# Kernel tuning notes

Measured on AMD Instinct MI355X. Metric: run time of the kernel, lower is better.

Reference implementation:

```python
import jax, jax.numpy as jnp
import numpy as np

EMBED_DIM = 1024
NUM_HEADS = 16
HEAD_DIM = EMBED_DIM // NUM_HEADS
SCALE = HEAD_DIM ** -0.5


def setup_inputs() -> dict:
    key = jax.random.key(0)
    ks = jax.random.split(key, 12)
    B, S, D = 4, 2048, EMBED_DIM
    s = 0.02
    return {
        "query": jax.random.normal(ks[0], (B, S, D), jnp.float32),
        "key": jax.random.normal(ks[1], (B, S, D), jnp.float32),
        "value": jax.random.normal(ks[2], (B, S, D), jnp.float32),
        "Wq": jax.random.normal(ks[3], (D, D), jnp.float32) * s,
        "bq": jnp.zeros((D,), jnp.float32),
        "Wk": jax.random.normal(ks[4], (D, D), jnp.float32) * s,
        "bk": jnp.zeros((D,), jnp.float32),
        "Wv": jax.random.normal(ks[5], (D, D), jnp.float32) * s,
        "bv": jnp.zeros((D,), jnp.float32),
        "Wo": jax.random.normal(ks[6], (D, D), jnp.float32) * s,
        "bo": jnp.zeros((D,), jnp.float32),
    }


def reference(query, key, value, Wq, bq, Wk, bk, Wv, bv, Wo, bo):
    B, S, D = query.shape
    H, Hd = NUM_HEADS, HEAD_DIM

    # Linear projections (torch Linear: x @ W^T + b)
    q = query @ Wq.T + bq
    k = key @ Wk.T + bk
    v = value @ Wv.T + bv

    # [B, H, S, Hd]
    q = q.reshape(B, S, H, Hd).transpose(0, 2, 1, 3)
    k = k.reshape(B, -1, H, Hd).transpose(0, 2, 1, 3)
    v = v.reshape(B, -1, H, Hd).transpose(0, 2, 1, 3)

    # scores: [B, H, S, Skv]
    scores = jnp.einsum("bhsd,bhtd->bhst", q, k) * SCALE

    # is_causal=True: mask strictly upper triangle
    Skv = k.shape[2]
    causal = jnp.triu(jnp.ones((S, Skv), dtype=bool), k=1)
    scores = jnp.where(causal, -jnp.inf, scores)

    attn = jax.nn.softmax(scores, axis=-1)
    out = jnp.einsum("bhst,bhtd->bhsd", attn, v)  # [B, H, S, Hd]
    out = out.transpose(0, 2, 1, 3).reshape(B, S, D)
    output = out @ Wo.T + bo

    # need_weights=True, average_attn_weights=True -> mean over heads
    attn_weights = attn.mean(axis=1)  # [B, S, Skv]
    return output, attn_weights
```

## Files before the change

kernel.cpp:

```cpp
#include <hip/hip_runtime.h>
#include <hip/hip_bf16.h>
#include <cmath>

#define BC     4
#define SEQ    2048
#define DMODEL 1024
#define NHEAD  16
#define HD     64
#define ASCALE 0.125f
#define LOG2E  1.44269504f

typedef __bf16 bf16x8 __attribute__((ext_vector_type(8)));
typedef __bf16 bf16x4 __attribute__((ext_vector_type(4)));
typedef float  f32x4  __attribute__((ext_vector_type(4)));

__device__ __forceinline__ f32x4 mfma16x16x32(bf16x8 a, bf16x8 b, f32x4 c) {
    return __builtin_amdgcn_mfma_f32_16x16x32_bf16(a, b, c, 0, 0, 0);
}

__device__ __forceinline__ float fexp2(float x) {
    return __builtin_amdgcn_exp2f(x);
}

__device__ __forceinline__ void gload_lds16(const __bf16* g, __bf16* l) {
    __builtin_amdgcn_global_load_lds(
        (const __attribute__((address_space(1))) void*)g,
        (__attribute__((address_space(3))) void*)l, 16, 0, 0);
}

__global__ __launch_bounds__(256) void cvt_qkv(const float* __restrict__ a,
                                               const float* __restrict__ b,
                                               const float* __restrict__ c,
                                               __bf16* __restrict__ oa,
                                               __bf16* __restrict__ ob,
                                               __bf16* __restrict__ oc) {
    const float* in; __bf16* out;
    if (blockIdx.y == 0)      { in = a; out = oa; }
    else if (blockIdx.y == 1) { in = b; out = ob; }
    else                      { in = c; out = oc; }
    const size_t i = ((size_t)blockIdx.x * 256 + threadIdx.x) * 8;
    float4 f0 = *(const float4*)(in + i);
    float4 f1 = *(const float4*)(in + i + 4);
    bf16x8 o;
    o[0] = (__bf16)f0.x; o[1] = (__bf16)f0.y; o[2] = (__bf16)f0.z; o[3] = (__bf16)f0.w;
    o[4] = (__bf16)f1.x; o[5] = (__bf16)f1.y; o[6] = (__bf16)f1.z; o[7] = (__bf16)f1.w;
    *(bf16x8*)(out + i) = o;
}

__global__ __launch_bounds__(256) void cvt_w(const float* __restrict__ a,
                                             const float* __restrict__ b,
                                             const float* __restrict__ c,
                                             const float* __restrict__ d,
                                             __bf16* __restrict__ oa,
                                             __bf16* __restrict__ ob,
                                             __bf16* __restrict__ oc,
                                             __bf16* __restrict__ od) {
    const float* in; __bf16* out;
    if (blockIdx.y == 0)      { in = a; out = oa; }
    else if (blockIdx.y == 1) { in = b; out = ob; }
    else if (blockIdx.y == 2) { in = c; out = oc; }
    else                      { in = d; out = od; }
    const size_t i = ((size_t)blockIdx.x * 256 + threadIdx.x) * 8;
    float4 f0 = *(const float4*)(in + i);
    float4 f1 = *(const float4*)(in + i + 4);
    bf16x8 o;
    o[0] = (__bf16)f0.x; o[1] = (__bf16)f0.y; o[2] = (__bf16)f0.z; o[3] = (__bf16)f0.w;
    o[4] = (__bf16)f1.x; o[5] = (__bf16)f1.y; o[6] = (__bf16)f1.z; o[7] = (__bf16)f1.w;
    *(bf16x8*)(out + i) = o;
}

template <typename TO, bool VT>
__global__ __launch_bounds__(256) void gemm_bt16(const __bf16* __restrict__ A,
                                                 const __bf16* __restrict__ W,
                                                 const float* __restrict__ bias,
                                                 TO* __restrict__ out,
                                                 float scale) {
    constexpr int K = DMODEL, N = DMODEL;
    __shared__ __bf16 As[128 * 64];
    __shared__ __bf16 Bs[128 * 64];
    const int tid = threadIdx.x;
    const int lane = tid & 63;
    const int wid = tid >> 6;
    const int lr = lane & 15;
    const int lg = lane >> 4;
    const int wr = (wid >> 1) * 64;
    const int wc = (wid & 1) * 64;
    const int bm = blockIdx.x * 128;
    const int bn = blockIdx.y * 128;

    f32x4 acc[4][4] = {};

    for (int k0 = 0; k0 < K; k0 += 64) {
        #pragma unroll
        for (int i = 0; i < 4; ++i) {
            const int p = tid + 256 * i;
            const int row = p >> 3, c = p & 7;
            const int csrc = ((c ^ (row & 7)) * 8);
            gload_lds16(A + (size_t)(bm + row) * K + k0 + csrc, &As[p * 8]);
            gload_lds16(W + (size_t)(bn + row) * K + k0 + csrc, &Bs[p * 8]);
        }
        __syncthreads();

        #pragma unroll
        for (int kk = 0; kk < 2; ++kk) {
            bf16x8 af[4], bfg[4];
            #pragma unroll
            for (int m = 0; m < 4; ++m) {
                const int row = wr + m * 16 + lr;
                af[m] = *(const bf16x8*)&As[row * 64 + ((kk * 4 + lg) ^ (row & 7)) * 8];
            }
            #pragma unroll
            for (int n = 0; n < 4; ++n) {
                const int row = wc + n * 16 + lr;
                bfg[n] = *(const bf16x8*)&Bs[row * 64 + ((kk * 4 + lg) ^ (row & 7)) * 8];
            }
            #pragma unroll
            for (int m = 0; m < 4; ++m)
                #pragma unroll
                for (int n = 0; n < 4; ++n)
                    acc[m][n] = mfma16x16x32(af[m], bfg[n], acc[m][n]);
        }
        __syncthreads();
    }

    #pragma unroll
    for (int n = 0; n < 4; ++n) {
        const int col = bn + wc + n * 16 + lr;
        const float bb = bias[col];
        #pragma unroll
        for (int m = 0; m < 4; ++m) {
            const int row0 = bm + wr + m * 16 + lg * 4;
            if constexpr (VT) {
                const int h = col >> 6, hd = col & 63;
                const int b = row0 >> 11, s = row0 & 2047;
                bf16x4 pk;
                #pragma unroll
                for (int r = 0; r < 4; ++r) pk[r] = (__bf16)((acc[m][n][r] + bb) * scale);
                *(bf16x4*)((__bf16*)out + (((size_t)b * NHEAD + h) * HD + hd) * SEQ + s) = pk;
            } else {
                #pragma unroll
                for (int r = 0; r < 4; ++r)
                    out[(size_t)(row0 + r) * N + col] = (TO)((acc[m][n][r] + bb) * scale);
            }
        }
    }
}

__global__ __launch_bounds__(256) void flash_fwd(const __bf16* __restrict__ q,
                                                 const __bf16* __restrict__ k,
                                                 const __bf16* __restrict__ vt,
                                                 __bf16* __restrict__ o,
                                                 float* __restrict__ mbuf,
                                                 float* __restrict__ lbuf) {
    __shared__ __bf16 Ks[2][64][64];
    __shared__ __bf16 Vs[2][64][64];
    __shared__ __bf16 Ps[4][16][64];
    const int tid = threadIdx.x;
    const int lane = tid & 63;
    const int wid = tid >> 6;
    const int lr = lane & 15;
    const int lg = lane >> 4;

    const int flat = blockIdx.x;
    const int slot = flat >> 3;
    const int group = (flat & 7) * 8 + (slot >> 5);
    const int b = group >> 4;
    const int h = group & 15;
    const int qt = 31 - (slot & 31);

    const int qr = qt * 64 + wid * 16;
    const int myq = qr + lr;

    bf16x8 qf0, qf1;
    {
        const __bf16* qp = q + (size_t)(b * SEQ + myq) * DMODEL + h * HD + lg * 8;
        qf0 = ((const bf16x8*)qp)[0];
        qf1 = *(const bf16x8*)(qp + 32);
    }

    float m_run = -INFINITY;
    float l_run = 0.f;
    f32x4 oacc[4] = {};

    const int srow = tid >> 2;
    const int sc = (tid & 3) * 2;
    const int swz0 = (sc ^ (srow & 7)) * 8;
    const int swz1 = ((sc + 1) ^ (srow & 7)) * 8;
    const int rsw = (lr & 7);
    const int nt = qt + 1;

    const __bf16* kbase = k + (size_t)(b * SEQ + srow) * DMODEL + h * HD + sc * 8;
    const __bf16* vbase = vt + ((size_t)(b * NHEAD + h) * HD + srow) * SEQ + sc * 8;

    {
        bf16x8 kr0 = ((const bf16x8*)kbase)[0];
        bf16x8 kr1 = *(const bf16x8*)(kbase + 8);
        bf16x8 vr0 = ((const bf16x8*)vbase)[0];
        bf16x8 vr1 = *(const bf16x8*)(vbase + 8);
        *(bf16x8*)&Ks[0][srow][swz0] = kr0;
        *(bf16x8*)&Ks[0][srow][swz1] = kr1;
        *(bf16x8*)&Vs[0][srow][swz0] = vr0;
        *(bf16x8*)&Vs[0][srow][swz1] = vr1;
    }
    __syncthreads();

    for (int t = 0; t < nt; ++t) {
        const int buf = t & 1;
        const bool pre = (t + 1 < nt);
        bf16x8 kr0, kr1, vr0, vr1;
        if (pre) {
            const __bf16* kp = kbase + (size_t)(t + 1) * 64 * DMODEL;
            kr0 = ((const bf16x8*)kp)[0];
            kr1 = *(const bf16x8*)(kp + 8);
            const __bf16* vp = vbase + (t + 1) * 64;
            vr0 = ((const bf16x8*)vp)[0];
            vr1 = *(const bf16x8*)(vp + 8);
        }

        f32x4 z[4];
        __builtin_amdgcn_s_setprio(1);
        #pragma unroll
        for (int ts = 0; ts < 4; ++ts) {
            bf16x8 kf0 = *(const bf16x8*)&Ks[buf][ts * 16 + lr][(lg ^ rsw) * 8];
            bf16x8 kf1 = *(const bf16x8*)&Ks[buf][ts * 16 + lr][((4 + lg) ^ rsw) * 8];
            f32x4 acc = {0.f, 0.f, 0.f, 0.f};
            acc = mfma16x16x32(kf0, qf0, acc);
            acc = mfma16x16x32(kf1, qf1, acc);
            z[ts] = acc;
        }
        __builtin_amdgcn_s_setprio(0);

        if (t == qt) {
            #pragma unroll
            for (int ts = 0; ts < 4; ++ts)
                #pragma unroll
                for (int r = 0; r < 4; ++r)
                    if (t * 64 + ts * 16 + lg * 4 + r > myq) z[ts][r] = -INFINITY;
        }

        float a0 = fmaxf(fmaxf(z[0][0], z[0][1]), z[0][2]);
        float a1 = fmaxf(fmaxf(z[0][3], z[1][0]), z[1][1]);
        float a2 = fmaxf(fmaxf(z[1][2], z[1][3]), z[2][0]);
        float a3 = fmaxf(fmaxf(z[2][1], z[2][2]), z[2][3]);
        float a4 = fmaxf(fmaxf(z[3][0], z[3][1]), z[3][2]);
        float a5 = z[3][3];
        float b0 = fmaxf(fmaxf(a0, a1), a2);
        float b1 = fmaxf(fmaxf(a3, a4), a5);
        float mt = fmaxf(b0, b1);
        mt = fmaxf(mt, __shfl_xor(mt, 16));
        mt = fmaxf(mt, __shfl_xor(mt, 32));

        if (!__all(mt <= m_run + 11.54f)) {
            const float mnew = fmaxf(m_run, mt);
            const float alpha = fexp2(m_run - mnew);
            #pragma unroll
            for (int r = 0; r < 4; ++r) {
                const float ar = __shfl(alpha, lg * 4 + r);
                #pragma unroll
                for (int hf = 0; hf < 4; ++hf) oacc[hf][r] *= ar;
            }
            l_run *= alpha;
            m_run = mnew;
        }

        float rsum = 0.f;
        #pragma unroll
        for (int ts = 0; ts < 4; ++ts) {
            bf16x4 pk;
            #pragma unroll
            for (int r = 0; r < 4; ++r) {
                float pv = fexp2(z[ts][r] - m_run);
                rsum += pv;
                pk[r] = (__bf16)pv;
            }
            *(bf16x4*)&Ps[wid][lr][((ts * 2 + (lg >> 1)) ^ rsw) * 8 + (lg & 1) * 4] = pk;
        }
        rsum += __shfl_xor(rsum, 16);
        rsum += __shfl_xor(rsum, 32);
        l_run += rsum;

        bf16x8 pf0 = *(const bf16x8*)&Ps[wid][lr][(lg ^ rsw) * 8];
        bf16x8 pf1 = *(const bf16x8*)&Ps[wid][lr][((4 + lg) ^ rsw) * 8];
        __builtin_amdgcn_s_setprio(1);
        #pragma unroll
        for (int hf = 0; hf < 4; ++hf) {
            bf16x8 vf0 = *(const bf16x8*)&Vs[buf][hf * 16 + lr][(lg ^ rsw) * 8];
            bf16x8 vf1 = *(const bf16x8*)&Vs[buf][hf * 16 + lr][((4 + lg) ^ rsw) * 8];
            oacc[hf] = mfma16x16x32(pf0, vf0, oacc[hf]);
            oacc[hf] = mfma16x16x32(pf1, vf1, oacc[hf]);
        }
        __builtin_amdgcn_s_setprio(0);

        if (pre) {
            *(bf16x8*)&Ks[buf ^ 1][srow][swz0] = kr0;
            *(bf16x8*)&Ks[buf ^ 1][srow][swz1] = kr1;
            *(bf16x8*)&Vs[buf ^ 1][srow][swz0] = vr0;
            *(bf16x8*)&Vs[buf ^ 1][srow][swz1] = vr1;
        }
        __syncthreads();
    }

    const float linv = 1.f / l_run;
    #pragma unroll
    for (int r = 0; r < 4; ++r) {
        const float li = __shfl(linv, lg * 4 + r);
        #pragma unroll
        for (int hf = 0; hf < 4; ++hf)
            o[(size_t)(b * SEQ + qr + lg * 4 + r) * DMODEL + h * HD + hf * 16 + lr] =
                (__bf16)(oacc[hf][r] * li);
    }
    if (lg == 0) {
        mbuf[((size_t)b * SEQ + myq) * NHEAD + h] = m_run;
        lbuf[((size_t)b * SEQ + myq) * NHEAD + h] = l_run;
    }
}

__global__ __launch_bounds__(256) void attn_weights(const __bf16* __restrict__ q,
                                                    const __bf16* __restrict__ k,
                                                    const float* __restrict__ mbuf,
                                                    const float* __restrict__ lbuf,
                                                    float* __restrict__ wout) {
    __shared__ __bf16 Ks[2][128][64];
    const int flat = blockIdx.x;
    const int xcd = flat & 7;
    const int slot = flat >> 3;
    const int gi = slot >> 5;
    const int st = slot & 31;
    const int b = gi & 3;
    const int t2 = (gi >> 2) ? (15 - xcd) : xcd;

    const int tid = threadIdx.x;
    const int lane = tid & 63;
    const int wid = tid >> 6;
    const int lr = lane & 15;
    const int lg = lane >> 4;
    const int myq = st * 64 + wid * 16 + lr;
    const int k0 = t2 * 128;

    float* wp = wout + (size_t)(b * SEQ + myq) * SEQ + k0 + lg * 4;

    if (2 * t2 > st) {
        const f32x4 zz = {0.f, 0.f, 0.f, 0.f};
        #pragma unroll
        for (int ts = 0; ts < 8; ++ts) *(f32x4*)(wp + ts * 16) = zz;
        return;
    }
    const bool needmask = (st <= 2 * t2 + 1);

    f32x4 rm[4], rl[4];
    {
        const float* mp = mbuf + ((size_t)b * SEQ + myq) * NHEAD;
        const float* lp = lbuf + ((size_t)b * SEQ + myq) * NHEAD;
        #pragma unroll
        for (int i = 0; i < 4; ++i) rm[i] = *(const f32x4*)(mp + i * 4);
        #pragma unroll
        for (int i = 0; i < 4; ++i) {
            f32x4 t = *(const f32x4*)(lp + i * 4);
            #pragma unroll
            for (int r = 0; r < 4; ++r) rl[i][r] = 1.f / (t[r] * (float)NHEAD);
        }
    }

    const int srow = tid >> 1;
    const int scb = (tid & 1) * 4;
    const int rsw = (lr & 7);
    const __bf16* krow = k + (size_t)(b * SEQ + k0 + srow) * DMODEL + scb * 8;
    const __bf16* qbase = q + (size_t)(b * SEQ + myq) * DMODEL + lg * 8;

    {
        bf16x8 kr[4];
        #pragma unroll
        for (int c = 0; c < 4; ++c) kr[c] = *(const bf16x8*)(krow + c * 8);
        #pragma unroll
        for (int c = 0; c < 4; ++c)
            *(bf16x8*)&Ks[0][srow][((scb + c) ^ (srow & 7)) * 8] = kr[c];
    }
    bf16x8 qna = ((const bf16x8*)qbase)[0];
    bf16x8 qnb = *(const bf16x8*)(qbase + 32);

    f32x4 wacc[8] = {};
    __syncthreads();

    #pragma unroll
    for (int h = 0; h < NHEAD; ++h) {
        const int cur = h & 1;
        bf16x8 kr[4];
        if (h + 1 < NHEAD) {
            const __bf16* kp = krow + (h + 1) * HD;
            #pragma unroll
            for (int c = 0; c < 4; ++c) kr[c] = *(const bf16x8*)(kp + c * 8);
        }
        const bf16x8 qf0 = qna, qf1 = qnb;
        if (h + 1 < NHEAD) {
            qna = *(const bf16x8*)(qbase + (h + 1) * HD);
            qnb = *(const bf16x8*)(qbase + (h + 1) * HD + 32);
        }
        const float rmh = rm[h >> 2][h & 3];
        const float rlh = rl[h >> 2][h & 3];

        #pragma unroll
        for (int ts = 0; ts < 8; ++ts) {
            bf16x8 kf0 = *(const bf16x8*)&Ks[cur][ts * 16 + lr][(lg ^ rsw) * 8];
            bf16x8 kf1 = *(const bf16x8*)&Ks[cur][ts * 16 + lr][((4 + lg) ^ rsw) * 8];
            f32x4 zz = {0.f, 0.f, 0.f, 0.f};
            zz = mfma16x16x32(kf0, qf0, zz);
            zz = mfma16x16x32(kf1, qf1, zz);
            if (needmask) {
                #pragma unroll
                for (int r = 0; r < 4; ++r) {
                    float e = 0.f;
                    if (k0 + ts * 16 + lg * 4 + r <= myq)
                        e = fexp2(zz[r] - rmh) * rlh;
                    wacc[ts][r] += e;
                }
            } else {
                #pragma unroll
                for (int r = 0; r < 4; ++r)
                    wacc[ts][r] += fexp2(zz[r] - rmh) * rlh;
            }
        }

        if (h + 1 < NHEAD) {
            #pragma unroll
            for (int c = 0; c < 4; ++c)
                *(bf16x8*)&Ks[cur ^ 1][srow][((scb + c) ^ (srow & 7)) * 8] = kr[c];
        }
        __syncthreads();
    }

    #pragma unroll
    for (int ts = 0; ts < 8; ++ts)
        *(f32x4*)(wp + ts * 16) = wacc[ts];
}

extern "C" void kernel_launch(void* const* d_in, const int* in_sizes, int n_in,
                              void* d_out, int out_size, void* d_ws, size_t ws_size,
                              hipStream_t stream) {
    const float* query = (const float*)d_in[0];
    const float* key_  = (const float*)d_in[1];
    const float* value = (const float*)d_in[2];
    const float* Wq = (const float*)d_in[3];
    const float* bq = (const float*)d_in[4];
    const float* Wk = (const float*)d_in[5];
    const float* bk = (const float*)d_in[6];
    const float* Wv = (const float*)d_in[7];
    const float* bv = (const float*)d_in[8];
    const float* Wo = (const float*)d_in[9];
    const float* bo = (const float*)d_in[10];
    float* out = (float*)d_out;

    const size_t nelem = (size_t)BC * SEQ * DMODEL;
    char* p = (char*)d_ws;
    const size_t mat = nelem * sizeof(__bf16);
    __bf16* qb  = (__bf16*)p; p += mat;
    __bf16* kb  = (__bf16*)p; p += mat;
    __bf16* vtb = (__bf16*)p; p += mat;
    __bf16* ob  = (__bf16*)p; p += mat;
    const size_t wmat = (size_t)DMODEL * DMODEL * sizeof(__bf16);
    __bf16* wqb = (__bf16*)p; p += wmat;
    __bf16* wkb = (__bf16*)p; p += wmat;
    __bf16* wvb = (__bf16*)p; p += wmat;
    __bf16* wob = (__bf16*)p; p += wmat;
    float* mb = (float*)p; p += (size_t)BC * NHEAD * SEQ * sizeof(float);
    float* lb = (float*)p; p += (size_t)BC * NHEAD * SEQ * sizeof(float);

    float* wout = out + nelem;
    __bf16* qc = (__bf16*)wout;
    __bf16* kc = qc + nelem;
    __bf16* vc = kc + nelem;

    cvt_qkv<<<dim3((unsigned)(nelem / 2048), 3), 256, 0, stream>>>(query, key_, value, qc, kc, vc);
    cvt_w<<<dim3(DMODEL * DMODEL / 2048, 4), 256, 0, stream>>>(Wq, Wk, Wv, Wo, wqb, wkb, wvb, wob);

    const int M = BC * SEQ;
    dim3 gg(M / 128, DMODEL / 128);
    gemm_bt16<__bf16, false><<<gg, 256, 0, stream>>>(qc, wqb, bq, qb, ASCALE * LOG2E);
    gemm_bt16<__bf16, false><<<gg, 256, 0, stream>>>(kc, wkb, bk, kb, 1.f);
    gemm_bt16<__bf16, true ><<<gg, 256, 0, stream>>>(vc, wvb, bv, vtb, 1.f);

    flash_fwd<<<dim3(2048), 256, 0, stream>>>(qb, kb, vtb, ob, mb, lb);
    gemm_bt16<float, false><<<gg, 256, 0, stream>>>(ob, wob, bo, out, 1.f);

    attn_weights<<<dim3(2048), 256, 0, stream>>>(qb, kb, mb, lb, wout);
}
```

Before: 280.9 us.

## Enlarge flash attention query tile to 128 rows with 8 waves per block

The flash attention kernel now processes 128 query rows per block using 512 threads (8 waves), so each K/V tile loaded into shared memory is reused by twice as many waves, and the grid is halved. Each thread now stages one 16-byte chunk per tile instead of two. Waves whose query rows end before the current key tile skip compute but still join the loads and barriers. This cuts global K/V traffic per query, at the cost of idle waves on the diagonal tiles and more barrier stalls with larger blocks.

After: 275.1 us. 1.02x faster.

```diff
diff --git a/kernel.cpp b/kernel.cpp
--- a/kernel.cpp
+++ b/kernel.cpp
@@ -146,7 +146,7 @@
     }
 }
 
-__global__ __launch_bounds__(256) void flash_fwd(const __bf16* __restrict__ q,
+__global__ __launch_bounds__(512) void flash_fwd(const __bf16* __restrict__ q,
                                                  const __bf16* __restrict__ k,
                                                  const __bf16* __restrict__ vt,
                                                  __bf16* __restrict__ o,
@@ -154,7 +154,7 @@
                                                  float* __restrict__ lbuf) {
     __shared__ __bf16 Ks[2][64][64];
     __shared__ __bf16 Vs[2][64][64];
-    __shared__ __bf16 Ps[4][16][64];
+    __shared__ __bf16 Ps[8][16][64];
     const int tid = threadIdx.x;
     const int lane = tid & 63;
     const int wid = tid >> 6;
@@ -162,14 +162,16 @@
     const int lg = lane >> 4;
 
     const int flat = blockIdx.x;
+    const int xcd = flat & 7;
     const int slot = flat >> 3;
-    const int group = (flat & 7) * 8 + (slot >> 5);
+    const int group = xcd * 8 + (slot >> 4);
     const int b = group >> 4;
     const int h = group & 15;
-    const int qt = 31 - (slot & 31);
-
-    const int qr = qt * 64 + wid * 16;
+    const int qt = 15 - (slot & 15);
+
+    const int qr = qt * 128 + wid * 16;
     const int myq = qr + lr;
+    const int dtile = qr >> 6;
 
     bf16x8 qf0, qf1;
     {
@@ -182,120 +184,111 @@
     float l_run = 0.f;
     f32x4 oacc[4] = {};
 
-    const int srow = tid >> 2;
-    const int sc = (tid & 3) * 2;
-    const int swz0 = (sc ^ (srow & 7)) * 8;
-    const int swz1 = ((sc + 1) ^ (srow & 7)) * 8;
+    const int srow = tid >> 3;
+    const int sc = tid & 7;
+    const int swz = (sc ^ (srow & 7)) * 8;
     const int rsw = (lr & 7);
-    const int nt = qt + 1;
+    const int nt = 2 * qt + 2;
 
     const __bf16* kbase = k + (size_t)(b * SEQ + srow) * DMODEL + h * HD + sc * 8;
     const __bf16* vbase = vt + ((size_t)(b * NHEAD + h) * HD + srow) * SEQ + sc * 8;
 
     {
-        bf16x8 kr0 = ((const bf16x8*)kbase)[0];
-        bf16x8 kr1 = *(const bf16x8*)(kbase + 8);
-        bf16x8 vr0 = ((const bf16x8*)vbase)[0];
-        bf16x8 vr1 = *(const bf16x8*)(vbase + 8);
-        *(bf16x8*)&Ks[0][srow][swz0] = kr0;
-        *(bf16x8*)&Ks[0][srow][swz1] = kr1;
-        *(bf16x8*)&Vs[0][srow][swz0] = vr0;
-        *(bf16x8*)&Vs[0][srow][swz1] = vr1;
+        bf16x8 kr = *(const bf16x8*)kbase;
+        bf16x8 vr = *(const bf16x8*)vbase;
+        *(bf16x8*)&Ks[0][srow][swz] = kr;
+        *(bf16x8*)&Vs[0][srow][swz] = vr;
     }
     __syncthreads();
 
     for (int t = 0; t < nt; ++t) {
         const int buf = t & 1;
         const bool pre = (t + 1 < nt);
-        bf16x8 kr0, kr1, vr0, vr1;
+        bf16x8 kr, vr;
         if (pre) {
-            const __bf16* kp = kbase + (size_t)(t + 1) * 64 * DMODEL;
-            kr0 = ((const bf16x8*)kp)[0];
-            kr1 = *(const bf16x8*)(kp + 8);
-            const __bf16* vp = vbase + (t + 1) * 64;
-            vr0 = ((const bf16x8*)vp)[0];
-            vr1 = *(const bf16x8*)(vp + 8);
-        }
-
-        f32x4 z[4];
-        __builtin_amdgcn_s_setprio(1);
-        #pragma unroll
-        for (int ts = 0; ts < 4; ++ts) {
-            bf16x8 kf0 = *(const bf16x8*)&Ks[buf][ts * 16 + lr][(lg ^ rsw) * 8];
-            bf16x8 kf1 = *(const bf16x8*)&Ks[buf][ts * 16 + lr][((4 + lg) ^ rsw) * 8];
-            f32x4 acc = {0.f, 0.f, 0.f, 0.f};
-            acc = mfma16x16x32(kf0, qf0, acc);
-            acc = mfma16x16x32(kf1, qf1, acc);
-            z[ts] = acc;
-        }
-        __builtin_amdgcn_s_setprio(0);
-
-        if (t == qt) {
-            #pragma unroll
-            for (int ts = 0; ts < 4; ++ts)
-                #pragma unroll
-                for (int r = 0; r < 4; ++r)
-                    if (t * 64 + ts * 16 + lg * 4 + r > myq) z[ts][r] = -INFINITY;
-        }
-
-        float a0 = fmaxf(fmaxf(z[0][0], z[0][1]), z[0][2]);
-        float a1 = fmaxf(fmaxf(z[0][3], z[1][0]), z[1][1]);
-        float a2 = fmaxf(fmaxf(z[1][2], z[1][3]), z[2][0]);
-        float a3 = fmaxf(fmaxf(z[2][1], z[2][2]), z[2][3]);
-        float a4 = fmaxf(fmaxf(z[3][0], z[3][1]), z[3][2]);
-        float a5 = z[3][3];
-        float b0 = fmaxf(fmaxf(a0, a1), a2);
-        float b1 = fmaxf(fmaxf(a3, a4), a5);
-        float mt = fmaxf(b0, b1);
-        mt = fmaxf(mt, __shfl_xor(mt, 16));
-        mt = fmaxf(mt, __shfl_xor(mt, 32));
-
-        if (!__all(mt <= m_run + 11.54f)) {
-            const float mnew = fmaxf(m_run, mt);
-            const float alpha = fexp2(m_run - mnew);
-            #pragma unroll
-            for (int r = 0; r < 4; ++r) {
-                const float ar = __shfl(alpha, lg * 4 + r);
-                #pragma unroll
-                for (int hf = 0; hf < 4; ++hf) oacc[hf][r] *= ar;
-            }
-            l_run *= alpha;
-            m_run = mnew;
-        }
-
-        float rsum = 0.f;
-        #pragma unroll
-        for (int ts = 0; ts < 4; ++ts) {
-            bf16x4 pk;
-            #pragma unroll
-            for (int r = 0; r < 4; ++r) {
-                float pv = fexp2(z[ts][r] - m_run);
-                rsum += pv;
-                pk[r] = (__bf16)pv;
-            }
-            *(bf16x4*)&Ps[wid][lr][((ts * 2 + (lg >> 1)) ^ rsw) * 8 + (lg & 1) * 4] = pk;
-        }
-        rsum += __shfl_xor(rsum, 16);
-        rsum += __shfl_xor(rsum, 32);
-        l_run += rsum;
-
-        bf16x8 pf0 = *(const bf16x8*)&Ps[wid][lr][(lg ^ rsw) * 8];
-        bf16x8 pf1 = *(const bf16x8*)&Ps[wid][lr][((4 + lg) ^ rsw) * 8];
-        __builtin_amdgcn_s_setprio(1);
-        #pragma unroll
-        for (int hf = 0; hf < 4; ++hf) {
-            bf16x8 vf0 = *(const bf16x8*)&Vs[buf][hf * 16 + lr][(lg ^ rsw) * 8];
-            bf16x8 vf1 = *(const bf16x8*)&Vs[buf][hf * 16 + lr][((4 + lg) ^ rsw) * 8];
-            oacc[hf] = mfma16x16x32(pf0, vf0, oacc[hf]);
-            oacc[hf] = mfma16x16x32(pf1, vf1, oacc[hf]);
-        }
-        __builtin_amdgcn_s_setprio(0);
+            kr = *(const bf16x8*)(kbase + (size_t)(t + 1) * 64 * DMODEL);
+            vr = *(const bf16x8*)(vbase + (t + 1) * 64);
+        }
+
+        if (t <= dtile) {
+            f32x4 z[4];
+            __builtin_amdgcn_s_setprio(1);
+            #pragma unroll
+            for (int ts = 0; ts < 4; ++ts) {
+                bf16x8 kf0 = *(const bf16x8*)&Ks[buf][ts * 16 + lr][(lg ^ rsw) * 8];
+                bf16x8 kf1 = *(const bf16x8*)&Ks[buf][ts * 16 + lr][((4 + lg) ^ rsw) * 8];
+                f32x4 acc = {0.f, 0.f, 0.f, 0.f};
+                acc = mfma16x16x32(kf0, qf0, acc);
+                acc = mfma16x16x32(kf1, qf1, acc);
+                z[ts] = acc;
+            }
+            __builtin_amdgcn_s_setprio(0);
+
+            if (t == dtile) {
+                #pragma unroll
+                for (int ts = 0; ts < 4; ++ts)
+                    #pragma unroll
+                    for (int r = 0; r < 4; ++r)
+                        if (t * 64 + ts * 16 + lg * 4 + r > myq) z[ts][r] = -INFINITY;
+            }
+
+            float a0 = fmaxf(fmaxf(z[0][0], z[0][1]), z[0][2]);
+            float a1 = fmaxf(fmaxf(z[0][3], z[1][0]), z[1][1]);
+            float a2 = fmaxf(fmaxf(z[1][2], z[1][3]), z[2][0]);
+            float a3 = fmaxf(fmaxf(z[2][1], z[2][2]), z[2][3]);
+            float a4 = fmaxf(fmaxf(z[3][0], z[3][1]), z[3][2]);
+            float a5 = z[3][3];
+            float b0 = fmaxf(fmaxf(a0, a1), a2);
+            float b1 = fmaxf(fmaxf(a3, a4), a5);
+            float mt = fmaxf(b0, b1);
+            mt = fmaxf(mt, __shfl_xor(mt, 16));
+            mt = fmaxf(mt, __shfl_xor(mt, 32));
+
+            if (!__all(mt <= m_run + 11.54f)) {
+                const float mnew = fmaxf(m_run, mt);
+                const float alpha = fexp2(m_run - mnew);
+                #pragma unroll
+                for (int r = 0; r < 4; ++r) {
+                    const float ar = __shfl(alpha, lg * 4 + r);
+                    #pragma unroll
+                    for (int hf = 0; hf < 4; ++hf) oacc[hf][r] *= ar;
+                }
+                l_run *= alpha;
+                m_run = mnew;
+            }
+
+            float rsum = 0.f;
+            #pragma unroll
+            for (int ts = 0; ts < 4; ++ts) {
+                bf16x4 pk;
+                #pragma unroll
+                for (int r = 0; r < 4; ++r) {
+                    float pv = fexp2(z[ts][r] - m_run);
+                    rsum += pv;
+                    pk[r] = (__bf16)pv;
+                }
+                *(bf16x4*)&Ps[wid][lr][((ts * 2 + (lg >> 1)) ^ rsw) * 8 + (lg & 1) * 4] = pk;
+            }
+            rsum += __shfl_xor(rsum, 16);
+            rsum += __shfl_xor(rsum, 32);
+            l_run += rsum;
+
+            bf16x8 pf0 = *(const bf16x8*)&Ps[wid][lr][(lg ^ rsw) * 8];
+            bf16x8 pf1 = *(const bf16x8*)&Ps[wid][lr][((4 + lg) ^ rsw) * 8];
+            __builtin_amdgcn_s_setprio(1);
+            #pragma unroll
+            for (int hf = 0; hf < 4; ++hf) {
+                bf16x8 vf0 = *(const bf16x8*)&Vs[buf][hf * 16 + lr][(lg ^ rsw) * 8];
+                bf16x8 vf1 = *(const bf16x8*)&Vs[buf][hf * 16 + lr][((4 + lg) ^ rsw) * 8];
+                oacc[hf] = mfma16x16x32(pf0, vf0, oacc[hf]);
+                oacc[hf] = mfma16x16x32(pf1, vf1, oacc[hf]);
+            }
+            __builtin_amdgcn_s_setprio(0);
+        }
 
         if (pre) {
-            *(bf16x8*)&Ks[buf ^ 1][srow][swz0] = kr0;
-            *(bf16x8*)&Ks[buf ^ 1][srow][swz1] = kr1;
-            *(bf16x8*)&Vs[buf ^ 1][srow][swz0] = vr0;
-            *(bf16x8*)&Vs[buf ^ 1][srow][swz1] = vr1;
+            *(bf16x8*)&Ks[buf ^ 1][srow][swz] = kr;
+            *(bf16x8*)&Vs[buf ^ 1][srow][swz] = vr;
         }
         __syncthreads();
     }
@@ -478,7 +471,7 @@
     gemm_bt16<__bf16, false><<<gg, 256, 0, stream>>>(kc, wkb, bk, kb, 1.f);
     gemm_bt16<__bf16, true ><<<gg, 256, 0, stream>>>(vc, wvb, bv, vtb, 1.f);
 
-    flash_fwd<<<dim3(2048), 256, 0, stream>>>(qb, kb, vtb, ob, mb, lb);
+    flash_fwd<<<dim3(1024), 512, 0, stream>>>(qb, kb, vtb, ob, mb, lb);
     gemm_bt16<float, false><<<gg, 256, 0, stream>>>(ob, wob, bo, out, 1.f);
 
     attn_weights<<<dim3(2048), 256, 0, stream>>>(qb, kb, mb, lb, wout);
```
